# Kernel tuning notes

Hardware: AMD Instinct MI355X
Metric: run time of the kernel (lower is better)

Reference implementation:

```python
import jax, jax.numpy as jnp
import numpy as np

N_NODES = 50000


def _sage_conv(x, src, dst, Wl, Wr, bl, num_nodes):
    # PyG SAGEConv (mean aggr): out = lin_l(mean_{j in N(i)} x_j) + lin_r(x_i)
    # messages flow src -> dst
    agg = jax.ops.segment_sum(x[src], dst, num_segments=num_nodes)          # [N, F]
    deg = jax.ops.segment_sum(jnp.ones_like(dst, dtype=x.dtype), dst,
                              num_segments=num_nodes)                       # [N]
    agg = agg / jnp.maximum(deg, 1.0)[:, None]
    return agg @ Wl + bl + x @ Wr


def setup_inputs() -> dict:
    key = jax.random.key(0)
    ks = jax.random.split(key, 9)
    F_in, H, C, E = 256, 256, 40, 800000
    s = lambda fan: 1.0 / np.sqrt(fan)
    x = jax.random.normal(ks[0], (N_NODES, F_in), dtype=jnp.float32)
    edge_index = jax.random.randint(ks[1], (2, E), 0, N_NODES, dtype=jnp.int32)
    W1l = jax.random.normal(ks[2], (F_in, H), dtype=jnp.float32) * s(F_in)
    W1r = jax.random.normal(ks[3], (F_in, H), dtype=jnp.float32) * s(F_in)
    b1 = jnp.zeros((H,), dtype=jnp.float32)
    W2l = jax.random.normal(ks[4], (H, C), dtype=jnp.float32) * s(H)
    W2r = jax.random.normal(ks[5], (H, C), dtype=jnp.float32) * s(H)
    b2 = jnp.zeros((C,), dtype=jnp.float32)
    Q = jax.random.normal(ks[6], (E // 2, C), dtype=jnp.float32) * s(E // 2)
    return {"x": x, "edge_index": edge_index, "W1l": W1l, "b1": b1,
            "W1r": W1r, "W2l": W2l, "b2": b2, "W2r": W2r, "Q": Q}


def reference(x, edge_index, W1l, b1, W1r, W2l, b2, W2r, Q):
    # Eval mode: F.dropout with training=False is identity.
    src, dst = edge_index[0], edge_index[1]
    h = _sage_conv(x, src, dst, W1l, W1r, b1, N_NODES)
    h = jax.nn.elu(h)
    out = _sage_conv(h, src, dst, W2l, W2r, b2, N_NODES)
    return (out, Q)
```

## Files before the change

### kernel.cpp

```cpp
#include <hip/hip_runtime.h>
#include <hip/hip_bf16.h>
#include <cstddef>

#define N_NODES 50000
#define M_PAD 50048
#define BSTRIDE 64

typedef __attribute__((ext_vector_type(8))) short short8;
typedef __attribute__((ext_vector_type(4))) float floatx4;

__device__ inline unsigned short f2bf(float f) {
    union { float f; unsigned u; } v; v.f = f;
    unsigned r = v.u + 0x7fff + ((v.u >> 16) & 1);
    return (unsigned short)(r >> 16);
}
__device__ inline float bfbits_lo(unsigned u) {
    union { unsigned u; float f; } v; v.u = u << 16; return v.f;
}
__device__ inline float bfbits_hi(unsigned u) {
    union { unsigned u; float f; } v; v.u = u & 0xffff0000u; return v.f;
}

__device__ inline void gload16(const void* g, void* l) {
    __builtin_amdgcn_global_load_lds(
        (const __attribute__((address_space(1))) unsigned int*)g,
        (__attribute__((address_space(3))) unsigned int*)l, 16, 0, 0);
}

#define PREP_NT (2048 * 256)
__global__ __launch_bounds__(256) void prep_count(
    const float* __restrict__ x,
    const float* __restrict__ W1l, const float* __restrict__ W1r,
    const float* __restrict__ W2l, const float* __restrict__ W2r,
    unsigned short* __restrict__ Abuf, unsigned short* __restrict__ B1t,
    unsigned short* __restrict__ B2t,
    const int* __restrict__ src, const int* __restrict__ dst,
    int* __restrict__ deg, int* __restrict__ bucket, int E) {
    int gtid = blockIdx.x * 256 + threadIdx.x;

    int e0 = gtid, e1 = gtid + PREP_NT;
    bool h0 = e0 < E, h1 = e1 < E;
    int d0 = 0, d1 = 0, s0 = 0, s1 = 0, r0 = 0, r1 = 0;
    if (h0) { d0 = dst[e0]; s0 = src[e0]; r0 = atomicAdd(&deg[d0], 1); }
    if (h1) { d1 = dst[e1]; s1 = src[e1]; r1 = atomicAdd(&deg[d1], 1); }

    for (int i = gtid; i < N_NODES * 32; i += PREP_NT) {
        int row = i >> 5;
        int c8 = i & 31;
        const float4* xp = reinterpret_cast<const float4*>(x + (size_t)row * 256 + c8 * 8);
        float4 v0 = xp[0], v1 = xp[1];
        uint4 o;
        o.x = (unsigned)f2bf(v0.x) | ((unsigned)f2bf(v0.y) << 16);
        o.y = (unsigned)f2bf(v0.z) | ((unsigned)f2bf(v0.w) << 16);
        o.z = (unsigned)f2bf(v1.x) | ((unsigned)f2bf(v1.y) << 16);
        o.w = (unsigned)f2bf(v1.z) | ((unsigned)f2bf(v1.w) << 16);
        *reinterpret_cast<uint4*>(Abuf + (size_t)row * 512 + 256 + c8 * 8) = o;
    }
    if (gtid < 256 * 512) {
        int n = gtid >> 9, k = gtid & 511;
        float v = (k < 256) ? W1l[(size_t)k * 256 + n] : W1r[(size_t)(k - 256) * 256 + n];
        B1t[(size_t)n * 512 + k] = f2bf(v);
    }
    if (gtid < 80 * 256) {
        int n = gtid >> 8, k = gtid & 255;
        float v = (n < 40) ? W2l[(size_t)k * 40 + n] : W2r[(size_t)k * 40 + (n - 40)];
        B2t[(size_t)n * 256 + k] = f2bf(v);
    }

    if (h0) bucket[(size_t)d0 * BSTRIDE + r0] = s0;
    if (h1) bucket[(size_t)d1 * BSTRIDE + r1] = s1;
}

__global__ __launch_bounds__(256) void aggregate1(
    const unsigned short* __restrict__ Abuf, const int* __restrict__ deg,
    const int* __restrict__ bucket,
    unsigned short* __restrict__ AbufOut, int N) {
    int node = blockIdx.x * 4 + (threadIdx.x >> 6);
    if (node >= N) return;
    int lane = threadIdx.x & 63;
    int half = lane >> 5;
    int dlane = lane & 31;
    const unsigned short* base = Abuf + 256 + (size_t)dlane * 8;
    const int* bkt = bucket + (size_t)node * BSTRIDE;
    int dg = deg[node];
    float a0 = 0.f, a1 = 0.f, a2 = 0.f, a3 = 0.f;
    float a4 = 0.f, a5 = 0.f, a6 = 0.f, a7 = 0.f;
    int k = half;
    for (; k + 15 < dg; k += 16) {
        uint4 v[8];
        #pragma unroll
        for (int u = 0; u < 8; ++u) {
            int j = bkt[k + u * 2];
            v[u] = *reinterpret_cast<const uint4*>(base + (size_t)j * 512);
        }
        #pragma unroll
        for (int u = 0; u < 8; ++u) {
            a0 += bfbits_lo(v[u].x); a1 += bfbits_hi(v[u].x);
            a2 += bfbits_lo(v[u].y); a3 += bfbits_hi(v[u].y);
            a4 += bfbits_lo(v[u].z); a5 += bfbits_hi(v[u].z);
            a6 += bfbits_lo(v[u].w); a7 += bfbits_hi(v[u].w);
        }
    }
    for (; k + 7 < dg; k += 8) {
        uint4 v[4];
        #pragma unroll
        for (int u = 0; u < 4; ++u) {
            int j = bkt[k + u * 2];
            v[u] = *reinterpret_cast<const uint4*>(base + (size_t)j * 512);
        }
        #pragma unroll
        for (int u = 0; u < 4; ++u) {
            a0 += bfbits_lo(v[u].x); a1 += bfbits_hi(v[u].x);
            a2 += bfbits_lo(v[u].y); a3 += bfbits_hi(v[u].y);
            a4 += bfbits_lo(v[u].z); a5 += bfbits_hi(v[u].z);
            a6 += bfbits_lo(v[u].w); a7 += bfbits_hi(v[u].w);
        }
    }
    for (; k < dg; k += 2) {
        int j = bkt[k];
        uint4 v = *reinterpret_cast<const uint4*>(base + (size_t)j * 512);
        a0 += bfbits_lo(v.x); a1 += bfbits_hi(v.x); a2 += bfbits_lo(v.y); a3 += bfbits_hi(v.y);
        a4 += bfbits_lo(v.z); a5 += bfbits_hi(v.z); a6 += bfbits_lo(v.w); a7 += bfbits_hi(v.w);
    }
    a0 += __shfl_xor(a0, 32, 64); a1 += __shfl_xor(a1, 32, 64);
    a2 += __shfl_xor(a2, 32, 64); a3 += __shfl_xor(a3, 32, 64);
    a4 += __shfl_xor(a4, 32, 64); a5 += __shfl_xor(a5, 32, 64);
    a6 += __shfl_xor(a6, 32, 64); a7 += __shfl_xor(a7, 32, 64);
    if (half == 0) {
        float s = 1.0f / (float)(dg > 1 ? dg : 1);
        uint4 w;
        w.x = (unsigned)f2bf(a0 * s) | ((unsigned)f2bf(a1 * s) << 16);
        w.y = (unsigned)f2bf(a2 * s) | ((unsigned)f2bf(a3 * s) << 16);
        w.z = (unsigned)f2bf(a4 * s) | ((unsigned)f2bf(a5 * s) << 16);
        w.w = (unsigned)f2bf(a6 * s) | ((unsigned)f2bf(a7 * s) << 16);
        *reinterpret_cast<uint4*>(AbufOut + (size_t)node * 512 + dlane * 8) = w;
    }
}

__global__ __launch_bounds__(256) void gemm1_mfma(
    const unsigned short* __restrict__ Abuf,
    const unsigned short* __restrict__ B1t,
    const float* __restrict__ bias,
    unsigned short* __restrict__ H,
    int M) {
    __shared__ unsigned short As[2][64 * 64];
    __shared__ unsigned short Bs[2][128 * 64];
    int tid = threadIdx.x;
    int row0 = blockIdx.y * 64;
    int bn = blockIdx.x;
    int wid = tid >> 6, lane = tid & 63;
    int wm = (wid >> 1) * 32;
    int wn = (wid & 1) * 64;
    int fr = lane & 15, fq = lane >> 4;

    int lrow8 = lane >> 3;
    int gco = ((lane & 7) ^ lrow8) * 8;
    const unsigned short* gA0 = Abuf + (size_t)(row0 + wid * 16 + 0 + lrow8) * 512 + gco;
    const unsigned short* gA1 = Abuf + (size_t)(row0 + wid * 16 + 8 + lrow8) * 512 + gco;
    const unsigned short* gB0 = B1t + (size_t)(bn * 128 + wid * 32 + 0  + lrow8) * 512 + gco;
    const unsigned short* gB1 = B1t + (size_t)(bn * 128 + wid * 32 + 8  + lrow8) * 512 + gco;
    const unsigned short* gB2 = B1t + (size_t)(bn * 128 + wid * 32 + 16 + lrow8) * 512 + gco;
    const unsigned short* gB3 = B1t + (size_t)(bn * 128 + wid * 32 + 24 + lrow8) * 512 + gco;

    floatx4 acc[2][4] = {};

    #define STAGE(buf, k0)                                       \
        gload16(gA0 + (k0), &As[buf][(wid * 16 + 0) * 64]);      \
        gload16(gA1 + (k0), &As[buf][(wid * 16 + 8) * 64]);      \
        gload16(gB0 + (k0), &Bs[buf][(wid * 32 + 0) * 64]);      \
        gload16(gB1 + (k0), &Bs[buf][(wid * 32 + 8) * 64]);      \
        gload16(gB2 + (k0), &Bs[buf][(wid * 32 + 16) * 64]);     \
        gload16(gB3 + (k0), &Bs[buf][(wid * 32 + 24) * 64]);

    #define COMPUTE(buf)                                                                  \
        {                                                                                 \
            _Pragma("unroll")                                                             \
            for (int kc = 0; kc < 2; ++kc) {                                              \
                short8 af[2], bfr[4];                                                     \
                _Pragma("unroll")                                                         \
                for (int mi = 0; mi < 2; ++mi) {                                          \
                    int row = wm + mi * 16 + fr;                                          \
                    af[mi] = *reinterpret_cast<const short8*>(                            \
                        &As[buf][row * 64 + (((kc * 4 + fq) ^ (fr & 7)) * 8)]);           \
                }                                                                         \
                _Pragma("unroll")                                                         \
                for (int ni = 0; ni < 4; ++ni) {                                          \
                    int row = wn + ni * 16 + fr;                                          \
                    bfr[ni] = *reinterpret_cast<const short8*>(                           \
                        &Bs[buf][row * 64 + (((kc * 4 + fq) ^ (fr & 7)) * 8)]);           \
                }                                                                         \
                _Pragma("unroll")                                                         \
                for (int mi = 0; mi < 2; ++mi)                                            \
                    _Pragma("unroll")                                                     \
                    for (int ni = 0; ni < 4; ++ni)                                        \
                        acc[mi][ni] = __builtin_amdgcn_mfma_f32_16x16x32_bf16(            \
                            af[mi], bfr[ni], acc[mi][ni], 0, 0, 0);                       \
            }                                                                             \
        }

    STAGE(0, 0);
    STAGE(1, 64);
    asm volatile("s_waitcnt vmcnt(6)" ::: "memory");
    __builtin_amdgcn_s_barrier();
    __builtin_amdgcn_sched_barrier(0);
    int cur = 0;
    #pragma unroll 1
    for (int t = 0; t < 6; ++t) {
        COMPUTE(cur);
        __builtin_amdgcn_sched_barrier(0);
        __builtin_amdgcn_s_barrier();
        STAGE(cur, (t + 2) * 64);
        asm volatile("s_waitcnt vmcnt(6)" ::: "memory");
        __builtin_amdgcn_s_barrier();
        __builtin_amdgcn_sched_barrier(0);
        cur ^= 1;
    }
    COMPUTE(cur);
    __builtin_amdgcn_sched_barrier(0);
    asm volatile("s_waitcnt vmcnt(0)" ::: "memory");
    __builtin_amdgcn_s_barrier();
    __builtin_amdgcn_sched_barrier(0);
    COMPUTE(cur ^ 1);
    #undef STAGE
    #undef COMPUTE

    #pragma unroll
    for (int ni = 0; ni < 4; ++ni) {
        int gcol = bn * 128 + wn + ni * 16 + fr;
        float bb = bias[gcol];
        #pragma unroll
        for (int mi = 0; mi < 2; ++mi) {
            #pragma unroll
            for (int r = 0; r < 4; ++r) {
                int grow = row0 + wm + mi * 16 + fq * 4 + r;
                float t = acc[mi][ni][r] + bb;
                t = (t > 0.f) ? t : expm1f(t);
                H[(size_t)grow * 256 + gcol] = f2bf(t);
            }
        }
    }
}

__global__ __launch_bounds__(256) void gemm2_mfma(
    const unsigned short* __restrict__ Hb,
    const unsigned short* __restrict__ B2t,
    const float* __restrict__ b2,
    unsigned short* __restrict__ Plb,
    float* __restrict__ Pr,
    int M) {
    __shared__ unsigned short Bsm[80 * 256];
    __shared__ unsigned short As[2][64 * 64];
    int tid = threadIdx.x;
    int row0 = blockIdx.x * 64;
    int wid = tid >> 6, lane = tid & 63;
    int wm = wid * 16;
    int fr = lane & 15, fq = lane >> 4;

    for (int c = tid; c < 2560; c += 256) {
        int n = c >> 5, ci = c & 31;
        short8 v = *reinterpret_cast<const short8*>(B2t + (size_t)n * 256 + ci * 8);
        *reinterpret_cast<short8*>(&Bsm[n * 256 + ((ci ^ (n & 7)) * 8)]) = v;
    }

    int lrow8 = lane >> 3;
    int gco = ((lane & 7) ^ lrow8) * 8;
    const unsigned short* gA0 = Hb + (size_t)(row0 + wid * 16 + 0 + lrow8) * 256 + gco;
    const unsigned short* gA1 = Hb + (size_t)(row0 + wid * 16 + 8 + lrow8) * 256 + gco;

    floatx4 acc[5] = {};

    #define STAGE2(buf, k0)                                      \
        gload16(gA0 + (k0), &As[buf][(wid * 16 + 0) * 64]);      \
        gload16(gA1 + (k0), &As[buf][(wid * 16 + 8) * 64]);

    #define COMPUTE2(buf, k0)                                                             \
        {                                                                                 \
            _Pragma("unroll")                                                             \
            for (int kc = 0; kc < 2; ++kc) {                                              \
                short8 af;                                                                \
                {                                                                         \
                    int row = wm + fr;                                                    \
                    af = *reinterpret_cast<const short8*>(                                \
                        &As[buf][row * 64 + (((kc * 4 + fq) ^ (fr & 7)) * 8)]);           \
                }                                                                         \
                _Pragma("unroll")                                                         \
                for (int ni = 0; ni < 5; ++ni) {                                          \
                    int n = ni * 16 + fr;                                                 \
                    int c = ((k0) >> 3) + kc * 4 + fq;                                    \
                    short8 bfr = *reinterpret_cast<const short8*>(                        \
                        &Bsm[n * 256 + ((c ^ (n & 7)) * 8)]);                             \
                    acc[ni] = __builtin_amdgcn_mfma_f32_16x16x32_bf16(                    \
                        af, bfr, acc[ni], 0, 0, 0);                                       \
                }                                                                         \
            }                                                                             \
        }

    STAGE2(0, 0);
    __syncthreads();
    int cur = 0;
    #pragma unroll 1
    for (int t = 0; t < 3; ++t) {
        STAGE2(cur ^ 1, (t + 1) * 64);
        COMPUTE2(cur, t * 64);
        __syncthreads();
        cur ^= 1;
    }
    COMPUTE2(cur, 192);
    #undef STAGE2
    #undef COMPUTE2

    #pragma unroll
    for (int r = 0; r < 4; ++r) {
        int grow = row0 + wm + fq * 4 + r;
        if (grow < M) {
            #pragma unroll
            for (int ni = 0; ni < 5; ++ni) {
                int col = ni * 16 + fr;
                float v = acc[ni][r];
                if (col < 40)
                    Plb[(size_t)grow * 40 + col] = f2bf(v);
                else
                    Pr[(size_t)grow * 40 + (col - 40)] = v + b2[col - 40];
            }
        }
    }
}

__global__ __launch_bounds__(256) void final_kernel(
    const unsigned short* __restrict__ Plb, const float* __restrict__ Pr,
    const int* __restrict__ deg, const int* __restrict__ bucket,
    float* __restrict__ out, int N) {
    int wv = blockIdx.x * 4 + (threadIdx.x >> 6);
    int lid = threadIdx.x & 63;
    int sub = lid / 20;
    if (sub >= 3) return;
    int node = wv * 3 + sub;
    if (node >= N) return;
    int lane = lid - sub * 20;
    const int* bkt = bucket + (size_t)node * BSTRIDE;
    int dg = deg[node];
    float s0 = 0.f, s1 = 0.f;
    int k = 0;
    for (; k + 4 <= dg; k += 4) {
        unsigned v0 = *reinterpret_cast<const unsigned*>(Plb + (size_t)bkt[k]     * 40 + lane * 2);
        unsigned v1 = *reinterpret_cast<const unsigned*>(Plb + (size_t)bkt[k + 1] * 40 + lane * 2);
        unsigned v2 = *reinterpret_cast<const unsigned*>(Plb + (size_t)bkt[k + 2] * 40 + lane * 2);
        unsigned v3 = *reinterpret_cast<const unsigned*>(Plb + (size_t)bkt[k + 3] * 40 + lane * 2);
        s0 += bfbits_lo(v0) + bfbits_lo(v1) + bfbits_lo(v2) + bfbits_lo(v3);
        s1 += bfbits_hi(v0) + bfbits_hi(v1) + bfbits_hi(v2) + bfbits_hi(v3);
    }
    for (; k < dg; ++k) {
        unsigned v = *reinterpret_cast<const unsigned*>(Plb + (size_t)bkt[k] * 40 + lane * 2);
        s0 += bfbits_lo(v);
        s1 += bfbits_hi(v);
    }
    float inv = 1.0f / (float)(dg > 1 ? dg : 1);
    float2 pr = *reinterpret_cast<const float2*>(Pr + (size_t)node * 40 + lane * 2);
    float2 o;
    o.x = s0 * inv + pr.x;
    o.y = s1 * inv + pr.y;
    *reinterpret_cast<float2*>(out + (size_t)node * 40 + lane * 2) = o;
}


extern "C" void kernel_launch(void* const* d_in, const int* in_sizes, int n_in,
                              void* d_out, int out_size, void* d_ws, size_t ws_size,
                              hipStream_t stream) {
    const float* x   = (const float*)d_in[0];
    const int*   ei  = (const int*)d_in[1];
    const float* W1l = (const float*)d_in[2];
    const float* b1  = (const float*)d_in[3];
    const float* W1r = (const float*)d_in[4];
    const float* W2l = (const float*)d_in[5];
    const float* b2  = (const float*)d_in[6];
    const float* W2r = (const float*)d_in[7];
    const float* Q   = (const float*)d_in[8];
    const int E = in_sizes[1] / 2;
    const int N = N_NODES;
    const int* src = ei;
    const int* dst = ei + E;

    unsigned short* Abuf = (unsigned short*)d_ws;
    unsigned short* h    = Abuf + (size_t)M_PAD * 512;
    unsigned short* B1t  = h + (size_t)M_PAD * 256;
    unsigned short* B2t  = B1t + 256 * 512;
    unsigned short* Plb  = B2t + 80 * 256;
    float* Pr      = (float*)(Plb + (size_t)N * 40 + 32);
    int*   deg     = (int*)(Pr + (size_t)N * 40);
    int*   bucket  = deg + N;

    float* out = (float*)d_out;

    hipMemsetAsync(deg, 0, sizeof(int) * (size_t)N, stream);
    prep_count<<<2048, 256, 0, stream>>>(x, W1l, W1r, W2l, W2r,
                                         Abuf, B1t, B2t, src, dst, deg, bucket, E);

    aggregate1<<<(N + 3) / 4, 256, 0, stream>>>(Abuf, deg, bucket, Abuf, N);

    gemm1_mfma<<<dim3(2, M_PAD / 64), 256, 0, stream>>>(Abuf, B1t, b1, h, N);
    gemm2_mfma<<<M_PAD / 64, 256, 0, stream>>>(h, B2t, b2, Plb, Pr, N);
    final_kernel<<<(N + 11) / 12, 256, 0, stream>>>(Plb, Pr, deg, bucket, out, N);

    hipMemcpyAsync(out + (size_t)N * 40, Q, sizeof(float) * (size_t)in_sizes[8],
                   hipMemcpyDeviceToDevice, stream);
}
```

Measured before the change: 221.5 us.

## Split first-layer aggregation by feature slice and store neighbor buckets as uint16

The first-layer neighbor aggregation now splits the 256 features into 8 column slices of 32, each handled by separate blocks. Each wave processes 8 consecutive nodes, and lanes gather 8-byte pieces of neighbor rows, so each slice's gathered working set is small enough to stay resident in cache. Neighbor-index buckets are stored as 16-bit values instead of 32-bit, halving index traffic; this relies on node ids staying below 65536. The tradeoff is that every bucket is now read once per slice, and each lane issues smaller loads with fewer in flight, which may reduce memory-level parallelism.

```diff
diff --git a/kernel.cpp b/kernel.cpp
--- a/kernel.cpp
+++ b/kernel.cpp
@@ -35,7 +35,7 @@
     unsigned short* __restrict__ Abuf, unsigned short* __restrict__ B1t,
     unsigned short* __restrict__ B2t,
     const int* __restrict__ src, const int* __restrict__ dst,
-    int* __restrict__ deg, int* __restrict__ bucket, int E) {
+    int* __restrict__ deg, unsigned short* __restrict__ bucket, int E) {
     int gtid = blockIdx.x * 256 + threadIdx.x;
 
     int e0 = gtid, e1 = gtid + PREP_NT;
@@ -67,73 +67,57 @@
         B2t[(size_t)n * 256 + k] = f2bf(v);
     }
 
-    if (h0) bucket[(size_t)d0 * BSTRIDE + r0] = s0;
-    if (h1) bucket[(size_t)d1 * BSTRIDE + r1] = s1;
+    if (h0) bucket[(size_t)d0 * BSTRIDE + r0] = (unsigned short)s0;
+    if (h1) bucket[(size_t)d1 * BSTRIDE + r1] = (unsigned short)s1;
 }
 
 __global__ __launch_bounds__(256) void aggregate1(
     const unsigned short* __restrict__ Abuf, const int* __restrict__ deg,
-    const int* __restrict__ bucket,
+    const unsigned short* __restrict__ bucket,
     unsigned short* __restrict__ AbufOut, int N) {
-    int node = blockIdx.x * 4 + (threadIdx.x >> 6);
-    if (node >= N) return;
+    int g = blockIdx.x & 7;
+    int chunk = blockIdx.x >> 3;
+    int wv = threadIdx.x >> 6;
     int lane = threadIdx.x & 63;
-    int half = lane >> 5;
-    int dlane = lane & 31;
-    const unsigned short* base = Abuf + 256 + (size_t)dlane * 8;
-    const int* bkt = bucket + (size_t)node * BSTRIDE;
-    int dg = deg[node];
-    float a0 = 0.f, a1 = 0.f, a2 = 0.f, a3 = 0.f;
-    float a4 = 0.f, a5 = 0.f, a6 = 0.f, a7 = 0.f;
-    int k = half;
-    for (; k + 15 < dg; k += 16) {
-        uint4 v[8];
-        #pragma unroll
-        for (int u = 0; u < 8; ++u) {
-            int j = bkt[k + u * 2];
-            v[u] = *reinterpret_cast<const uint4*>(base + (size_t)j * 512);
-        }
-        #pragma unroll
-        for (int u = 0; u < 8; ++u) {
-            a0 += bfbits_lo(v[u].x); a1 += bfbits_hi(v[u].x);
-            a2 += bfbits_lo(v[u].y); a3 += bfbits_hi(v[u].y);
-            a4 += bfbits_lo(v[u].z); a5 += bfbits_hi(v[u].z);
-            a6 += bfbits_lo(v[u].w); a7 += bfbits_hi(v[u].w);
-        }
-    }
-    for (; k + 7 < dg; k += 8) {
-        uint4 v[4];
-        #pragma unroll
-        for (int u = 0; u < 4; ++u) {
-            int j = bkt[k + u * 2];
-            v[u] = *reinterpret_cast<const uint4*>(base + (size_t)j * 512);
-        }
-        #pragma unroll
-        for (int u = 0; u < 4; ++u) {
-            a0 += bfbits_lo(v[u].x); a1 += bfbits_hi(v[u].x);
-            a2 += bfbits_lo(v[u].y); a3 += bfbits_hi(v[u].y);
-            a4 += bfbits_lo(v[u].z); a5 += bfbits_hi(v[u].z);
-            a6 += bfbits_lo(v[u].w); a7 += bfbits_hi(v[u].w);
-        }
-    }
-    for (; k < dg; k += 2) {
-        int j = bkt[k];
-        uint4 v = *reinterpret_cast<const uint4*>(base + (size_t)j * 512);
-        a0 += bfbits_lo(v.x); a1 += bfbits_hi(v.x); a2 += bfbits_lo(v.y); a3 += bfbits_hi(v.y);
-        a4 += bfbits_lo(v.z); a5 += bfbits_hi(v.z); a6 += bfbits_lo(v.w); a7 += bfbits_hi(v.w);
-    }
-    a0 += __shfl_xor(a0, 32, 64); a1 += __shfl_xor(a1, 32, 64);
-    a2 += __shfl_xor(a2, 32, 64); a3 += __shfl_xor(a3, 32, 64);
-    a4 += __shfl_xor(a4, 32, 64); a5 += __shfl_xor(a5, 32, 64);
-    a6 += __shfl_xor(a6, 32, 64); a7 += __shfl_xor(a7, 32, 64);
-    if (half == 0) {
-        float s = 1.0f / (float)(dg > 1 ? dg : 1);
-        uint4 w;
-        w.x = (unsigned)f2bf(a0 * s) | ((unsigned)f2bf(a1 * s) << 16);
-        w.y = (unsigned)f2bf(a2 * s) | ((unsigned)f2bf(a3 * s) << 16);
-        w.z = (unsigned)f2bf(a4 * s) | ((unsigned)f2bf(a5 * s) << 16);
-        w.w = (unsigned)f2bf(a6 * s) | ((unsigned)f2bf(a7 * s) << 16);
-        *reinterpret_cast<uint4*>(AbufOut + (size_t)node * 512 + dlane * 8) = w;
+    int sub = lane >> 3;
+    int off = lane & 7;
+    const unsigned short* base = Abuf + 256 + g * 32 + off * 4;
+    int node0 = chunk * 32 + wv * 8;
+    for (int ni = 0; ni < 8; ++ni) {
+        int node = node0 + ni;
+        if (node >= N) break;
+        const unsigned short* bkt = bucket + (size_t)node * BSTRIDE;
+        int dg = deg[node];
+        float a0 = 0.f, a1 = 0.f, a2 = 0.f, a3 = 0.f;
+        int k = sub;
+        for (; k + 8 < dg; k += 16) {
+            int j0 = bkt[k], j1 = bkt[k + 8];
+            uint2 v0 = *reinterpret_cast<const uint2*>(base + (size_t)j0 * 512);
+            uint2 v1 = *reinterpret_cast<const uint2*>(base + (size_t)j1 * 512);
+            a0 += bfbits_lo(v0.x) + bfbits_lo(v1.x);
+            a1 += bfbits_hi(v0.x) + bfbits_hi(v1.x);
+            a2 += bfbits_lo(v0.y) + bfbits_lo(v1.y);
+            a3 += bfbits_hi(v0.y) + bfbits_hi(v1.y);
+        }
+        if (k < dg) {
+            int j = bkt[k];
+            uint2 v = *reinterpret_cast<const uint2*>(base + (size_t)j * 512);
+            a0 += bfbits_lo(v.x); a1 += bfbits_hi(v.x);
+            a2 += bfbits_lo(v.y); a3 += bfbits_hi(v.y);
+        }
+        a0 += __shfl_xor(a0, 8, 64);  a1 += __shfl_xor(a1, 8, 64);
+        a2 += __shfl_xor(a2, 8, 64);  a3 += __shfl_xor(a3, 8, 64);
+        a0 += __shfl_xor(a0, 16, 64); a1 += __shfl_xor(a1, 16, 64);
+        a2 += __shfl_xor(a2, 16, 64); a3 += __shfl_xor(a3, 16, 64);
+        a0 += __shfl_xor(a0, 32, 64); a1 += __shfl_xor(a1, 32, 64);
+        a2 += __shfl_xor(a2, 32, 64); a3 += __shfl_xor(a3, 32, 64);
+        if (sub == 0) {
+            float s = 1.0f / (float)(dg > 1 ? dg : 1);
+            uint2 w;
+            w.x = (unsigned)f2bf(a0 * s) | ((unsigned)f2bf(a1 * s) << 16);
+            w.y = (unsigned)f2bf(a2 * s) | ((unsigned)f2bf(a3 * s) << 16);
+            *reinterpret_cast<uint2*>(AbufOut + (size_t)node * 512 + g * 32 + off * 4) = w;
+        }
     }
 }
 
@@ -328,7 +312,7 @@
 
 __global__ __launch_bounds__(256) void final_kernel(
     const unsigned short* __restrict__ Plb, const float* __restrict__ Pr,
-    const int* __restrict__ deg, const int* __restrict__ bucket,
+    const int* __restrict__ deg, const unsigned short* __restrict__ bucket,
     float* __restrict__ out, int N) {
     int wv = blockIdx.x * 4 + (threadIdx.x >> 6);
     int lid = threadIdx.x & 63;
@@ -337,7 +321,7 @@
     int node = wv * 3 + sub;
     if (node >= N) return;
     int lane = lid - sub * 20;
-    const int* bkt = bucket + (size_t)node * BSTRIDE;
+    const unsigned short* bkt = bucket + (size_t)node * BSTRIDE;
     int dg = deg[node];
     float s0 = 0.f, s1 = 0.f;
     int k = 0;
@@ -387,7 +371,7 @@
     unsigned short* Plb  = B2t + 80 * 256;
     float* Pr      = (float*)(Plb + (size_t)N * 40 + 32);
     int*   deg     = (int*)(Pr + (size_t)N * 40);
-    int*   bucket  = deg + N;
+    unsigned short* bucket = (unsigned short*)(deg + N);
 
     float* out = (float*)d_out;
 
@@ -395,7 +379,8 @@
     prep_count<<<2048, 256, 0, stream>>>(x, W1l, W1r, W2l, W2r,
                                          Abuf, B1t, B2t, src, dst, deg, bucket, E);
 
-    aggregate1<<<(N + 3) / 4, 256, 0, stream>>>(Abuf, deg, bucket, Abuf, N);
+    const int nchunks = (N + 31) / 32;
+    aggregate1<<<nchunks * 8, 256, 0, stream>>>(Abuf, deg, bucket, Abuf, N);
 
     gemm1_mfma<<<dim3(2, M_PAD / 64), 256, 0, stream>>>(Abuf, B1t, b1, h, N);
     gemm2_mfma<<<M_PAD / 64, 256, 0, stream>>>(h, B2t, b2, Plb, Pr, N);
```

New measurement: 273.5 us. +23.5%, slower.
